# Kernel tuning notes

Measured on AMD Instinct MI355X. Metric: run time of the kernel, lower is better.

## Reference

```python
import jax, jax.numpy as jnp
jax.config.update("jax_enable_x64", True)
import numpy as np

_SQRT2_MANT = 1865452045155277  # mantissa bits of sqrt(2), as in the torch module
_NAN_BITS = 0x7FF8000000000000
_INF_BITS = 0x7FF0000000000000
_MANT_MASK = 0xFFFFFFFFFFFFF
_ITERS = 12


def _bit_shifts():
    # MSB-first bit positions 63..0
    return jnp.uint64(63) - jnp.arange(64, dtype=jnp.uint64)


def _pack_bits(pulses):
    # [..., 64] {0,1} float pulses (MSB first) -> uint64
    w = jnp.uint64(1) << _bit_shifts()
    return jnp.sum((pulses > 0.5).astype(jnp.uint64) * w, axis=-1)


def _unpack_bits(u):
    # uint64 -> [..., 64] float32 pulses (MSB first)
    return ((u[..., None] >> _bit_shifts()) & jnp.uint64(1)).astype(jnp.float32)


def _sqrt_forward(x):
    u = _pack_bits(x)
    f = jax.lax.bitcast_convert_type(u, jnp.float64)

    # ---- SpikeFP64SqrtGuess: y0 = 2^floor(E/2) * (sqrt(2) mantissa if E odd else 1.0) ----
    e_x = ((u >> jnp.uint64(52)) & jnp.uint64(0x7FF)).astype(jnp.int64)
    e_real = e_x - 1023                      # 11-bit two's-complement adder in torch
    is_odd = (e_real & 1) == 1               # LSB of two's complement = parity
    e_new = ((e_real >> 1) + 1023).astype(jnp.uint64)  # sign-extended shift = floor div 2
    mant = jnp.where(is_odd, jnp.uint64(_SQRT2_MANT), jnp.uint64(0))
    y = jax.lax.bitcast_convert_type((e_new << jnp.uint64(52)) | mant, jnp.float64)

    # ---- 12 Newton-Raphson iterations: y = 0.5 * (y + x / y) in IEEE fp64 ----
    for _ in range(_ITERS):
        y = 0.5 * (y + f / y)

    # ---- special-case muxes, applied in the same order as the torch module ----
    s = (u >> jnp.uint64(63)) & jnp.uint64(1)
    m_any = (u & jnp.uint64(_MANT_MASK)) != 0
    e_all_one = e_x == 0x7FF
    e_is_zero = e_x == 0
    is_nan = e_all_one & m_any
    is_pos_inf = e_all_one & (~m_any) & (s == 0)
    is_zero = e_is_zero & (~m_any)
    is_neg = s == 1

    r = jax.lax.bitcast_convert_type(y, jnp.uint64)
    r = jnp.where(is_neg, jnp.uint64(_NAN_BITS), r)
    r = jnp.where(is_nan, jnp.uint64(_NAN_BITS), r)
    r = jnp.where(is_pos_inf, jnp.uint64(_INF_BITS), r)
    r = jnp.where(is_zero, jnp.uint64(0), r)
    return _unpack_bits(r)


def setup_inputs() -> dict:
    key = jax.random.key(0)
    k1, k2 = jax.random.split(key)
    N = 1 << 20  # 1048576 fp64 values as bit pulses
    # random positive normal doubles: exponent in [1, 2046], random 52-bit mantissa
    e = jax.random.randint(k1, (N,), 1, 2047, dtype=jnp.int64).astype(jnp.uint64)
    m = jax.random.randint(k2, (N,), 0, 1 << 52, dtype=jnp.int64).astype(jnp.uint64)
    bits = (e << jnp.uint64(52)) | m
    x = _unpack_bits(bits)  # [N, 64] float32 pulses
    return {"x": x}


def reference(x) -> jnp.ndarray:
    return _sqrt_forward(x)
```

## Files before the change

### kernel.cpp

```cpp
#include <hip/hip_runtime.h>
#include <cstdint>


#pragma clang fp contract(off)

static constexpr uint64_t kSqrt2Mant = 1865452045155277ULL;
static constexpr uint64_t kNanBits   = 0x7FF8000000000000ULL;
static constexpr uint64_t kInfBits   = 0x7FF0000000000000ULL;
static constexpr uint64_t kMantMask  = 0xFFFFFFFFFFFFFULL;

__global__ __launch_bounds__(256) void spike_fp64_sqrt_kernel(
    const float* __restrict__ x, float* __restrict__ out, int rows) {
  const int lane   = threadIdx.x & 63;
  const int waveId = (int)blockIdx.x * 4 + (threadIdx.x >> 6);
  const long long waveRow0 = (long long)waveId * 64;
  const int col = lane ^ 63;

  uint64_t u = 0;
  const bool fullWave = (waveRow0 + 64) <= (long long)rows;
  if (fullWave) {
    const float* base = x + waveRow0 * 64 + col;
#pragma unroll
    for (int b = 0; b < 2; ++b) {
      float v[32];
#pragma unroll
      for (int k = 0; k < 32; ++k) v[k] = base[(b * 32 + k) * 64];
#pragma unroll
      for (int k = 0; k < 32; ++k) {
        unsigned long long m = __ballot(v[k] > 0.5f);
        if (lane == b * 32 + k) u = m;
      }
    }
  } else {
#pragma unroll
    for (int rr = 0; rr < 64; ++rr) {
      const long long row = waveRow0 + rr;
      float v = (row < (long long)rows) ? x[row * 64 + col] : 0.0f;
      unsigned long long m = __ballot(v > 0.5f);
      if (lane == rr) u = m;
    }
  }

  const double f = __longlong_as_double((long long)u);

  const int e_x    = (int)((u >> 52) & 0x7FF);
  const int e_real = e_x - 1023;
  const long long e_half = ((long long)e_real) >> 1;
  const uint64_t mant = ((e_real & 1) != 0) ? kSqrt2Mant : 0ULL;
  const uint64_t ybits = (((uint64_t)(e_half + 1023)) << 52) | mant;
  double y = __longlong_as_double((long long)ybits);

#pragma unroll
  for (int it = 0; it < 12; ++it) {
    y = 0.5 * (y + f / y);
  }

  uint64_t r = (uint64_t)__double_as_longlong(y);
  const bool is_neg    = (u >> 63) != 0;
  const bool m_any     = (u & kMantMask) != 0;
  const bool e_all_one = (e_x == 0x7FF);
  const bool e_is_zero = (e_x == 0);
  if (is_neg) r = kNanBits;
  if (e_all_one && m_any) r = kNanBits;
  if (e_all_one && !m_any && !is_neg) r = kInfBits;
  if (e_is_zero && !m_any) r = 0ULL;

  const long long rl = (long long)r;
#pragma unroll
  for (int j = 0; j < 16; ++j) {
    const int srcRow = 4 * j + (lane >> 4);
    const uint64_t b = (uint64_t)__shfl(rl, srcRow, 64);
    const int c0 = (lane & 15) * 4;
    float4 o;
    o.x = (float)((b >> (63 - c0)) & 1ULL);
    o.y = (float)((b >> (62 - c0)) & 1ULL);
    o.z = (float)((b >> (61 - c0)) & 1ULL);
    o.w = (float)((b >> (60 - c0)) & 1ULL);
    const long long row = waveRow0 + srcRow;
    if (row < (long long)rows) {
      *reinterpret_cast<float4*>(out + row * 64 + c0) = o;
    }
  }
}

extern "C" void kernel_launch(void* const* d_in, const int* in_sizes, int n_in,
                              void* d_out, int out_size, void* d_ws, size_t ws_size,
                              hipStream_t stream) {
  const float* x = (const float*)d_in[0];
  float* out = (float*)d_out;
  const int rows = in_sizes[0] / 64;
  const int rowsPerBlock = 256;
  const int grid = (rows + rowsPerBlock - 1) / rowsPerBlock;
  spike_fp64_sqrt_kernel<<<grid, 256, 0, stream>>>(x, out, rows);
}
```

Before: 430.2 us.

## Split sqrt kernel into separate pack/compute and unpack kernels via workspace

Splits the single fused kernel in two. The first kernel reads the pulse bits, runs the Newton iterations and writes 64-bit words to a workspace. The second kernel reads those words and expands them back into float pulses. Input loads also switch to nontemporal loads. The split may let the store-heavy expansion overlap better or use the hardware more evenly, but it adds a second launch and a workspace round trip of 8 bytes per row.

```diff
diff --git a/kernel.cpp b/kernel.cpp
--- a/kernel.cpp
+++ b/kernel.cpp
@@ -4,13 +4,15 @@
 
 #pragma clang fp contract(off)
 
+typedef float f32x4 __attribute__((ext_vector_type(4)));
+
 static constexpr uint64_t kSqrt2Mant = 1865452045155277ULL;
 static constexpr uint64_t kNanBits   = 0x7FF8000000000000ULL;
 static constexpr uint64_t kInfBits   = 0x7FF0000000000000ULL;
 static constexpr uint64_t kMantMask  = 0xFFFFFFFFFFFFFULL;
 
-__global__ __launch_bounds__(256) void spike_fp64_sqrt_kernel(
-    const float* __restrict__ x, float* __restrict__ out, int rows) {
+__global__ __launch_bounds__(256) void spike_sqrt_pack_kernel(
+    const float* __restrict__ x, uint64_t* __restrict__ w, int rows) {
   const int lane   = threadIdx.x & 63;
   const int waveId = (int)blockIdx.x * 4 + (threadIdx.x >> 6);
   const long long waveRow0 = (long long)waveId * 64;
@@ -24,7 +26,8 @@
     for (int b = 0; b < 2; ++b) {
       float v[32];
 #pragma unroll
-      for (int k = 0; k < 32; ++k) v[k] = base[(b * 32 + k) * 64];
+      for (int k = 0; k < 32; ++k)
+        v[k] = __builtin_nontemporal_load(base + (size_t)(b * 32 + k) * 64);
 #pragma unroll
       for (int k = 0; k < 32; ++k) {
         unsigned long long m = __ballot(v[k] > 0.5f);
@@ -32,7 +35,7 @@
       }
     }
   } else {
-#pragma unroll
+#pragma unroll 4
     for (int rr = 0; rr < 64; ++rr) {
       const long long row = waveRow0 + rr;
       float v = (row < (long long)rows) ? x[row * 64 + col] : 0.0f;
@@ -65,20 +68,33 @@
   if (e_all_one && !m_any && !is_neg) r = kInfBits;
   if (e_is_zero && !m_any) r = 0ULL;
 
+  const long long myRow = waveRow0 + lane;
+  if (myRow < (long long)rows) w[myRow] = r;
+}
+
+__global__ __launch_bounds__(256) void spike_unpack_kernel(
+    const uint64_t* __restrict__ w, float* __restrict__ out, int rows) {
+  const int lane   = threadIdx.x & 63;
+  const int waveId = (int)blockIdx.x * 4 + (threadIdx.x >> 6);
+  const long long waveRow0 = (long long)waveId * 64;
+
+  const long long myRow = waveRow0 + lane;
+  const uint64_t r = (myRow < (long long)rows) ? w[myRow] : 0ULL;
   const long long rl = (long long)r;
+
 #pragma unroll
-  for (int j = 0; j < 16; ++j) {
-    const int srcRow = 4 * j + (lane >> 4);
+  for (int t = 0; t < 16; ++t) {
+    const int srcRow = 4 * t + (lane >> 4);
     const uint64_t b = (uint64_t)__shfl(rl, srcRow, 64);
     const int c0 = (lane & 15) * 4;
-    float4 o;
+    f32x4 o;
     o.x = (float)((b >> (63 - c0)) & 1ULL);
     o.y = (float)((b >> (62 - c0)) & 1ULL);
     o.z = (float)((b >> (61 - c0)) & 1ULL);
     o.w = (float)((b >> (60 - c0)) & 1ULL);
     const long long row = waveRow0 + srcRow;
     if (row < (long long)rows) {
-      *reinterpret_cast<float4*>(out + row * 64 + c0) = o;
+      *reinterpret_cast<f32x4*>(out + row * 64 + c0) = o;
     }
   }
 }
@@ -88,8 +104,10 @@
                               hipStream_t stream) {
   const float* x = (const float*)d_in[0];
   float* out = (float*)d_out;
+  uint64_t* words = (uint64_t*)d_ws;
   const int rows = in_sizes[0] / 64;
   const int rowsPerBlock = 256;
   const int grid = (rows + rowsPerBlock - 1) / rowsPerBlock;
-  spike_fp64_sqrt_kernel<<<grid, 256, 0, stream>>>(x, out, rows);
+  spike_sqrt_pack_kernel<<<grid, 256, 0, stream>>>(x, words, rows);
+  spike_unpack_kernel<<<grid, 256, 0, stream>>>(words, out, rows);
 }
```

Result: faster. 419.7 us (-2.4%).
